# Performance work log

Measured on AMD Instinct MI355X. Metric: run time of the kernel, lower is better.

## Reference

```python
import jax, jax.numpy as jnp
import numpy as np

EPS_BN = 1e-5  # torch BatchNorm1d default eps


def setup_inputs() -> dict:
    key = jax.random.key(0)
    k1, k2, k3 = jax.random.split(key, 3)
    B, C, L = 512, 8, 16384
    attn_maps = jax.random.normal(k1, (B, C, L), dtype=jnp.float32)
    target_matrix = jax.random.uniform(k2, (B, C, C), dtype=jnp.float32)
    conv_bias = jnp.ones((C,), dtype=jnp.float32) * 0.5  # nn.Parameter(torch.ones(8)/2)
    w_fc = jax.random.normal(k3, (3, 1), dtype=jnp.float32) * 0.1
    b_fc = jnp.zeros((3,), dtype=jnp.float32)
    return {"attn_maps": attn_maps, "target_matrix": target_matrix,
            "conv_bias": conv_bias, "w_fc": w_fc, "b_fc": b_fc}


def reference(attn_maps, target_matrix, conv_bias, w_fc, b_fc):
    B, C, L = attn_maps.shape  # C == 8 (fixed by the grouped 1x1 conv)
    # (attn - mean of per-row means) * 100; rows are uniform length so this is the global mean
    x = (attn_maps - jnp.mean(attn_maps)) * 100.0
    # grouped conv1d, kernel 1, weight == 5: per-channel affine, then sigmoid / 5
    bin_maps = jax.nn.sigmoid(5.0 * x + conv_bias[None, :, None]) / 5.0  # (B, C, L)
    b5 = bin_maps * 5.0
    # vectorized triangular IoU: intersection / union over the length dim
    inter = jnp.einsum('bil,bjl->bij', b5, b5)                     # (B, C, C)
    union = L - jnp.einsum('bil,bjl->bij', 1.0 - b5, 1.0 - b5)      # (B, C, C)
    tril = jnp.tril(jnp.ones((C, C), dtype=bool))
    sim = jnp.where(tril, inter / union, 0.0)
    # rep_type 'abs': sum of |sim - 100*target| over the lower triangle (incl. diag)
    tm = target_matrix * 100.0
    st = jnp.sum(jnp.where(tril, jnp.abs(sim - tm), 0.0), axis=(1, 2))  # (B,)
    # BatchNorm1d(1, affine=False) in training mode: normalize over the batch
    mu = jnp.mean(st)
    var = jnp.var(st)  # biased variance, as torch BN uses for normalization
    st_n = (st - mu) * jax.lax.rsqrt(var + EPS_BN)                  # (B,)
    # final linear 1 -> 3 (original Linear(128,3) is shape-inconsistent; see notes)
    out = st_n[:, None] @ w_fc.T + b_fc                              # (B, 3)
    return out
```

## Files before the change

kernel.cpp:

```cpp
#include <hip/hip_runtime.h>
#include <math.h>

typedef float f32x4 __attribute__((ext_vector_type(4)));
typedef _Float16 f16x2 __attribute__((ext_vector_type(2)));

#define B_DIM 512
#define C_DIM 8
#define L_DIM 16384
#define NELEM (B_DIM * C_DIM * L_DIM)
#define LOG2E 1.4426950408889634f
#define KA (-500.0f * LOG2E)

#if __has_builtin(__builtin_amdgcn_exp2f)
#define EXP2F __builtin_amdgcn_exp2f
#else
#define EXP2F exp2f
#endif

#if __has_builtin(__builtin_amdgcn_fdot2)
#define HAVE_FDOT2 1
#else
#define HAVE_FDOT2 0
#endif

#define H_NODE 0.25
#define F_P 1.2840254166877414f
#define F_M 0.7788007830714049f

#define TRI(i, j) ((i) * ((i) + 1) / 2 + (j))

#define WS_GRAM_OFF 8192

__global__ __launch_bounds__(256) void k_main(const f32x4* __restrict__ in4,
                                              const float* __restrict__ bias,
                                              float* __restrict__ asum,
                                              float* __restrict__ gram_t) {
  const int tid = threadIdx.x;
  const int lane = tid & 63, wv = tid >> 6;
  const int nodesel = tid >> 7;
  const int pt = tid & 127;
  const int b = blockIdx.x;

  const float Fn = nodesel ? F_M : F_P;
  float kc[C_DIM];
#pragma unroll
  for (int c = 0; c < C_DIM; ++c) kc[c] = bias[c] * (-LOG2E);

  float acc[44];
#pragma unroll
  for (int k = 0; k < 44; ++k) acc[k] = 0.f;
  float asacc = 0.f;

#if HAVE_FDOT2
  const f16x2 ONE2 = {(_Float16)1.f, (_Float16)1.f};
#endif

  const f32x4* base = in4 + (size_t)b * (C_DIM * 4096) + pt;

#pragma unroll 1
  for (int it = 0; it < 32; ++it) {
    f32x4 v[C_DIM];
#pragma unroll
    for (int c = 0; c < C_DIM; ++c) v[c] = base[c * 4096 + it * 128];
#pragma unroll
    for (int p = 0; p < 2; ++p) {
      float sx[C_DIM], sy[C_DIM];
#if HAVE_FDOT2
      f16x2 s2[C_DIM];
#endif
#pragma unroll
      for (int c = 0; c < C_DIM; ++c) {
        const float ax = p ? v[c].z : v[c].x;
        const float ay = p ? v[c].w : v[c].y;
        if (nodesel == 0) asacc += ax + ay;
        const float Ex = EXP2F(fmaf(KA, ax, kc[c]));
        const float Ey = EXP2F(fmaf(KA, ay, kc[c]));
        sx[c] = __builtin_amdgcn_rcpf(fmaf(Ex, Fn, 1.f));
        sy[c] = __builtin_amdgcn_rcpf(fmaf(Ey, Fn, 1.f));
#if HAVE_FDOT2
        s2[c] = __builtin_bit_cast(f16x2, __builtin_amdgcn_cvt_pkrtz(sx[c], sy[c]));
        acc[c] = __builtin_amdgcn_fdot2(s2[c], ONE2, acc[c], false);
#else
        acc[c] += sx[c] + sy[c];
#endif
      }
#pragma unroll
      for (int i = 0; i < C_DIM; ++i)
#pragma unroll
        for (int j = 0; j <= i; ++j) {
#if HAVE_FDOT2
          acc[8 + TRI(i, j)] =
              __builtin_amdgcn_fdot2(s2[i], s2[j], acc[8 + TRI(i, j)], false);
#else
          acc[8 + TRI(i, j)] =
              fmaf(sx[i], sx[j], fmaf(sy[i], sy[j], acc[8 + TRI(i, j)]));
#endif
        }
    }
  }

  __shared__ float lgr[4][44];
  __shared__ float las[2];
#pragma unroll
  for (int k = 0; k < 44; ++k) {
    float x = acc[k];
#pragma unroll
    for (int off = 32; off; off >>= 1) x += __shfl_xor(x, off, 64);
    if (lane == 0) lgr[wv][k] = x;
  }
  if (nodesel == 0) {
    float x = asacc;
#pragma unroll
    for (int off = 32; off; off >>= 1) x += __shfl_xor(x, off, 64);
    if (lane == 0) las[wv] = x;
  }
  __syncthreads();
  if (tid < 88) {
    const int n = tid / 44, k = tid - n * 44;
    gram_t[(size_t)(n * 44 + k) * 512 + b] = lgr[2 * n][k] + lgr[2 * n + 1][k];
  }
  if (tid == 96) asum[b] = las[0] + las[1];
}

__global__ __launch_bounds__(512) void k_final(const float* __restrict__ asum,
                                               const float* __restrict__ gram_t,
                                               const float* __restrict__ target,
                                               const float* __restrict__ w_fc,
                                               const float* __restrict__ b_fc,
                                               float* __restrict__ out) {
  const int t = threadIdx.x;
  __shared__ double red[512];

  red[t] = (double)asum[t];
  __syncthreads();
  for (int off = 256; off; off >>= 1) {
    if (t < off) red[t] += red[t + off];
    __syncthreads();
  }
  const double th = 500.0 * (red[0] / (double)NELEM);
  __syncthreads();

  const double w0 = (th + H_NODE) / (2.0 * H_NODE);
  const double w1 = (H_NODE - th) / (2.0 * H_NODE);

  const float* g = gram_t + t;
  double S[8], T[36];
#pragma unroll
  for (int i = 0; i < 8; ++i)
    S[i] = w0 * (double)g[(0 + i) * 512] + w1 * (double)g[(44 + i) * 512];
#pragma unroll
  for (int k = 0; k < 36; ++k)
    T[k] = w0 * (double)g[(8 + k) * 512] + w1 * (double)g[(52 + k) * 512];

  double st = 0.0;
#pragma unroll
  for (int i = 0; i < 8; ++i)
#pragma unroll
    for (int j = 0; j <= i; ++j) {
      double inter = T[TRI(i, j)];
      double uni = (S[i] + S[j]) - inter;
      double sim = inter / uni;
      double tm = 100.0 * (double)target[t * 64 + i * 8 + j];
      st += fabs(sim - tm);
    }

  red[t] = st;
  __syncthreads();
  for (int off = 256; off; off >>= 1) {
    if (t < off) red[t] += red[t + off];
    __syncthreads();
  }
  const double mean = red[0] * (1.0 / 512.0);
  __syncthreads();
  const double dd = st - mean;
  red[t] = dd * dd;
  __syncthreads();
  for (int off = 256; off; off >>= 1) {
    if (t < off) red[t] += red[t + off];
    __syncthreads();
  }
  const double var = red[0] * (1.0 / 512.0);
  const float stn = (float)((st - mean) / sqrt(var + 1e-5));
#pragma unroll
  for (int k = 0; k < 3; ++k)
    out[t * 3 + k] = fmaf(stn, w_fc[k], b_fc[k]);
}

extern "C" void kernel_launch(void* const* d_in, const int* in_sizes, int n_in,
                              void* d_out, int out_size, void* d_ws, size_t ws_size,
                              hipStream_t stream) {
  const float* attn   = (const float*)d_in[0];
  const float* target = (const float*)d_in[1];
  const float* bias   = (const float*)d_in[2];
  const float* w_fc   = (const float*)d_in[3];
  const float* b_fc   = (const float*)d_in[4];
  float* out = (float*)d_out;
  float* ws  = (float*)d_ws;

  float* asum   = ws;
  float* gram_t = ws + WS_GRAM_OFF;

  k_main<<<B_DIM, 256, 0, stream>>>((const f32x4*)attn, bias, asum, gram_t);
  k_final<<<1, 512, 0, stream>>>(asum, gram_t, target, w_fc, b_fc, out);
}
```

Measured before the change: 86.75 us.

## Triple-buffer input through LDS with async global_load_lds prefetch

Replaces direct per-thread global vector loads in the main kernel with asynchronous global-to-LDS loads into a three-stage shared-memory ring. Loads are issued three iterations ahead and gated with explicit vmcnt waits and barriers, so memory latency overlaps the exp/rcp/dot compute. The cost is 48KB of LDS per block, which can limit occupancy, plus two block barriers per iteration.

Result: faster. 81.39 us (-6.2%).

```diff
diff --git a/kernel.cpp b/kernel.cpp
--- a/kernel.cpp
+++ b/kernel.cpp
@@ -30,6 +30,12 @@
 #define TRI(i, j) ((i) * ((i) + 1) / 2 + (j))
 
 #define WS_GRAM_OFF 8192
+
+typedef const __attribute__((address_space(1))) unsigned int gu32_t;
+typedef __attribute__((address_space(3))) unsigned int lu32_t;
+__device__ __forceinline__ void gload_lds16(const void* g, void* l) {
+  __builtin_amdgcn_global_load_lds((gu32_t*)g, (lu32_t*)l, 16, 0, 0);
+}
 
 __global__ __launch_bounds__(256) void k_main(const f32x4* __restrict__ in4,
                                               const float* __restrict__ bias,
@@ -41,6 +47,8 @@
   const int pt = tid & 127;
   const int b = blockIdx.x;
 
+  __shared__ char smem[49152];
+
   const float Fn = nodesel ? F_M : F_P;
   float kc[C_DIM];
 #pragma unroll
@@ -55,13 +63,19 @@
   const f16x2 ONE2 = {(_Float16)1.f, (_Float16)1.f};
 #endif
 
-  const f32x4* base = in4 + (size_t)b * (C_DIM * 4096) + pt;
-
-#pragma unroll 1
-  for (int it = 0; it < 32; ++it) {
-    f32x4 v[C_DIM];
-#pragma unroll
-    for (int c = 0; c < C_DIM; ++c) v[c] = base[c * 4096 + it * 128];
+  const size_t gbase = (size_t)b * (C_DIM * 4096);
+
+  auto stage = [&](int it, int d) {
+#pragma unroll
+    for (int k = 0; k < 4; ++k) {
+      const int c = 2 * k + (tid >> 7);
+      const f32x4* g = in4 + gbase + (size_t)c * 4096 + it * 128 + pt;
+      char* l = smem + d * 16384 + k * 4096 + wv * 1024;
+      gload_lds16((const void*)g, (void*)l);
+    }
+  };
+
+  auto compute = [&](const f32x4* v) {
 #pragma unroll
     for (int p = 0; p < 2; ++p) {
       float sx[C_DIM], sy[C_DIM];
@@ -97,7 +111,37 @@
 #endif
         }
     }
-  }
+  };
+
+  auto consume = [&](int d) {
+    const char* lb = smem + d * 16384;
+    f32x4 v[C_DIM];
+#pragma unroll
+    for (int c = 0; c < C_DIM; ++c)
+      v[c] = *(const f32x4*)(lb + (c >> 1) * 4096 + (c & 1) * 2048 + pt * 16);
+    compute(v);
+  };
+
+  stage(0, 0);
+  stage(1, 1);
+  stage(2, 2);
+
+#pragma unroll 1
+  for (int it = 0; it < 30; ++it) {
+    const int d = it % 3;
+    asm volatile("s_waitcnt vmcnt(8)" ::: "memory");
+    __builtin_amdgcn_s_barrier();
+    consume(d);
+    __builtin_amdgcn_s_barrier();
+    if (it < 29) stage(it + 3, d);
+  }
+  asm volatile("s_waitcnt vmcnt(4)" ::: "memory");
+  __builtin_amdgcn_s_barrier();
+  consume(0);
+  __builtin_amdgcn_s_barrier();
+  asm volatile("s_waitcnt vmcnt(0)" ::: "memory");
+  __builtin_amdgcn_s_barrier();
+  consume(1);
 
   __shared__ float lgr[4][44];
   __shared__ float las[2];
```
